# Kernel optimization log

Hardware: AMD Instinct MI355X
Metric: run time of the kernel (lower is better)

## Reference

```python
import jax, jax.numpy as jnp
import numpy as np

FP8_MAX = 448.0  # max finite value of float8_e4m3fn


def setup_inputs() -> dict:
    key = jax.random.key(0)
    k1, k2, k3 = jax.random.split(key, 3)
    B, S, D_IN, D_OUT = 2, 4096, 2048, 8192
    x = jax.random.normal(k1, (B, S, D_IN), dtype=jnp.float32)
    # Weight is stored pre-quantized in fp8 (per-tensor scale), layout (in, out)
    w_fp32 = jax.random.normal(k2, (D_IN, D_OUT), dtype=jnp.float32) * 0.02
    weight_scale = jnp.float32(jnp.max(jnp.abs(w_fp32)) / FP8_MAX)
    weight = jnp.clip(w_fp32 / weight_scale, -FP8_MAX, FP8_MAX).astype(jnp.float8_e4m3fn)
    input_scale = jnp.float32(0.05)  # static per-tensor activation scale
    bias = jax.random.normal(k3, (D_OUT,), dtype=jnp.float32)
    return {"x": x, "weight": weight, "weight_scale": weight_scale,
            "input_scale": input_scale, "bias": bias}


def reference(x, weight, weight_scale, input_scale, bias):
    # static_quantize_e4m3_per_tensor: q = cast_fp8(clip(x / s)), returns (q, s)
    q = jnp.clip(x / input_scale, -FP8_MAX, FP8_MAX).astype(jnp.float8_e4m3fn)
    q2d = q.reshape(-1, q.shape[-1]).astype(jnp.float32)  # [B*S, D_in]
    w = weight.astype(jnp.float32)                         # [D_in, D_out]
    # cublas_scaled_mm: (q @ w) * scale_a * scale_b, out in x.dtype
    out = jnp.matmul(q2d, w) * (input_scale * weight_scale)
    out = out.astype(x.dtype) + bias.astype(x.dtype)
    return out.reshape(x.shape[:-1] + (out.shape[-1],))
```

## Files before the change

kernel.cpp:

```cpp
#include <hip/hip_runtime.h>

typedef __attribute__((ext_vector_type(4))) float floatx4;
typedef __attribute__((ext_vector_type(8))) int   intx8;

__device__ __forceinline__ unsigned int pack4_fp8(float f0, float f1, float f2, float f3) {
    int v = __builtin_amdgcn_cvt_pk_fp8_f32(f0, f1, 0, false);
    v = __builtin_amdgcn_cvt_pk_fp8_f32(f2, f3, v, true);
    return (unsigned int)v;
}

__device__ __forceinline__ void gload16(const unsigned char* g, unsigned char* l) {
    __builtin_amdgcn_global_load_lds(
        (const __attribute__((address_space(1))) unsigned int*)g,
        (__attribute__((address_space(3))) unsigned int*)l, 16, 0, 0);
}

__global__ void detect_kernel(const unsigned int* __restrict__ W, int* __restrict__ flag) {
    __shared__ int ok[2];
    if (threadIdx.x == 0) { ok[0] = 1; ok[1] = 1; }
    __syncthreads();
    int f32ok = 1, bf16ok = 1;
#pragma unroll
    for (int i = 0; i < 16; ++i) {
        unsigned int w = W[threadIdx.x * 16 + i];
        if (w & 0x000FFFFFu) f32ok = 0;
        if (w & 0x000F000Fu) bf16ok = 0;
    }
    if (!f32ok)  atomicAnd(&ok[0], 0);
    if (!bf16ok) atomicAnd(&ok[1], 0);
    __syncthreads();
    if (threadIdx.x == 0) *flag = ok[0] ? 2 : (ok[1] ? 1 : 0);
}

__global__ void quant_kernel(const float* __restrict__ x,
                             unsigned int* __restrict__ q,
                             const float* __restrict__ iscale, int n8) {
    int i = blockIdx.x * blockDim.x + threadIdx.x;
    if (i >= n8) return;
    float s = iscale[0];
    const float4* xv = (const float4*)x;
    float4 a = xv[2 * i];
    float4 b = xv[2 * i + 1];
    float v[8] = {a.x, a.y, a.z, a.w, b.x, b.y, b.z, b.w};
#pragma unroll
    for (int j = 0; j < 8; ++j) {
        float t = v[j] / s;
        v[j] = fminf(fmaxf(t, -448.0f), 448.0f);
    }
    q[2 * i]     = pack4_fp8(v[0], v[1], v[2], v[3]);
    q[2 * i + 1] = pack4_fp8(v[4], v[5], v[6], v[7]);
}

template <int MODE>
__device__ __forceinline__ void ingest_body(const unsigned char* __restrict__ W,
                                            unsigned char* __restrict__ Wt,
                                            int K, int N,
                                            unsigned char (*tile)[68]) {
    const int k0 = blockIdx.y * 64;
    const int n0 = blockIdx.x * 64;
    const int t = threadIdx.x;
    const int kr = t >> 2;
    const int cg = (t & 3) * 16;
    const size_t eidx = (size_t)(k0 + kr) * N + (n0 + cg);

    unsigned int w4[4];
    if constexpr (MODE == 0) {
        uint4 v = *(const uint4*)(W + eidx);
        w4[0] = v.x; w4[1] = v.y; w4[2] = v.z; w4[3] = v.w;
    } else if constexpr (MODE == 1) {
        const uint4* p = (const uint4*)((const unsigned short*)W + eidx);
        uint4 A0 = p[0], A1 = p[1];
        unsigned int uw[8] = {A0.x, A0.y, A0.z, A0.w, A1.x, A1.y, A1.z, A1.w};
#pragma unroll
        for (int g = 0; g < 4; ++g) {
            float f0 = __uint_as_float((uw[2 * g] & 0xFFFFu) << 16);
            float f1 = __uint_as_float((uw[2 * g] >> 16) << 16);
            float f2 = __uint_as_float((uw[2 * g + 1] & 0xFFFFu) << 16);
            float f3 = __uint_as_float((uw[2 * g + 1] >> 16) << 16);
            w4[g] = pack4_fp8(f0, f1, f2, f3);
        }
    } else {
        const float4* p = (const float4*)((const float*)W + eidx);
#pragma unroll
        for (int g = 0; g < 4; ++g) {
            float4 f = p[g];
            w4[g] = pack4_fp8(f.x, f.y, f.z, f.w);
        }
    }
#pragma unroll
    for (int g = 0; g < 4; ++g)
        *(unsigned int*)&tile[kr][cg + 4 * g] = w4[g];
    __syncthreads();

    const int nr = t >> 2;
    const int kg = (t & 3) * 16;
    uint4 o;
    unsigned int w[4];
#pragma unroll
    for (int g = 0; g < 4; ++g) {
        unsigned int b0 = tile[kg + g * 4 + 0][nr];
        unsigned int b1 = tile[kg + g * 4 + 1][nr];
        unsigned int b2 = tile[kg + g * 4 + 2][nr];
        unsigned int b3 = tile[kg + g * 4 + 3][nr];
        w[g] = b0 | (b1 << 8) | (b2 << 16) | (b3 << 24);
    }
    o.x = w[0]; o.y = w[1]; o.z = w[2]; o.w = w[3];
    *(uint4*)(Wt + (size_t)(n0 + nr) * K + k0 + kg) = o;
}

__global__ void ingest_kernel(const unsigned char* __restrict__ W,
                              unsigned char* __restrict__ Wt,
                              const int* __restrict__ flag, int K, int N) {
    __shared__ __align__(16) unsigned char tile[64][68];
    const int mode = *flag;
    if (mode == 0)      ingest_body<0>(W, Wt, K, N, tile);
    else if (mode == 1) ingest_body<1>(W, Wt, K, N, tile);
    else                ingest_body<2>(W, Wt, K, N, tile);
}

__global__ __launch_bounds__(256, 2) void gemm_mxfp8_kernel(
    const unsigned char* __restrict__ A,
    const unsigned char* __restrict__ Bt,
    float* __restrict__ C,
    const float* __restrict__ bias,
    const float* __restrict__ wscale,
    const float* __restrict__ iscale,
    int M, int N, int K) {
    __shared__ __align__(16) unsigned char As[2][16384];
    __shared__ __align__(16) unsigned char Bs[2][16384];

    const int tid  = threadIdx.x;
    const int lane = tid & 63;
    const int wv   = tid >> 6;
    const int wm   = wv >> 1;
    const int wn   = wv & 1;
    const int r16  = lane & 15;
    const int cq   = lane >> 4;

    const int nbx  = gridDim.x;
    const int nwg  = nbx * gridDim.y;
    const int orig = blockIdx.y * nbx + blockIdx.x;
    const int cpx  = nwg >> 3;
    const int swz  = (orig & 7) * cpx + (orig >> 3);
    const int bm   = (swz / nbx) * 128;
    const int bn   = (swz % nbx) * 128;

    const unsigned char* ga[4];
    const unsigned char* gb[4];
    int lo[4];
#pragma unroll
    for (int j = 0; j < 4; ++j) {
        const int u   = wv * 4 + j;
        const int rb  = u >> 1;
        const int rg  = u & 1;
        const int row = rb * 16 + r16;
        const int col = cq * 32 + rg * 16;
        ga[j] = A  + (size_t)(bm + row) * K + col;
        gb[j] = Bt + (size_t)(bn + row) * K + col;
        lo[j] = rb * 2048 + rg * 1024;
    }

    floatx4 acc[4][4] = {};

#pragma unroll
    for (int j = 0; j < 4; ++j) {
        gload16(ga[j], &As[0][lo[j]]);
        gload16(gb[j], &Bs[0][lo[j]]);
        ga[j] += 128; gb[j] += 128;
    }
    __syncthreads();

    const unsigned char* pa0 = &As[0][wm * 4 * 2048 + lane * 16];
    const unsigned char* pb0 = &Bs[0][wn * 4 * 2048 + lane * 16];

    union U8 { intx8 v; uint4 q[2]; };
    const int NT = K >> 7;
    int cur = 0;
    for (int kt = 0; kt < NT; ++kt) {
        if (kt + 1 < NT) {
#pragma unroll
            for (int j = 0; j < 4; ++j) {
                gload16(ga[j], &As[cur ^ 1][lo[j]]);
                gload16(gb[j], &Bs[cur ^ 1][lo[j]]);
                ga[j] += 128; gb[j] += 128;
            }
        }
        intx8 af[4], bf[4];
#pragma unroll
        for (int i = 0; i < 4; ++i) {
            U8 ua, ub;
            const unsigned char* qa = pa0 + cur * 16384 + i * 2048;
            const unsigned char* qb = pb0 + cur * 16384 + i * 2048;
            ua.q[0] = *(const uint4*)qa;
            ua.q[1] = *(const uint4*)(qa + 1024);
            ub.q[0] = *(const uint4*)qb;
            ub.q[1] = *(const uint4*)(qb + 1024);
            af[i] = ua.v;
            bf[i] = ub.v;
        }
#pragma unroll
        for (int im = 0; im < 4; ++im)
#pragma unroll
            for (int in = 0; in < 4; ++in)
                acc[im][in] = __builtin_amdgcn_mfma_scale_f32_16x16x128_f8f6f4(
                    af[im], bf[in], acc[im][in],
                    0, 0,
                    0, 0x7F7F7F7F,
                    0, 0x7F7F7F7F);
        __syncthreads();
        cur ^= 1;
    }
    (void)M;

    const float scale = iscale[0] * wscale[0];
    const int row0 = bm + wm * 64 + (cq << 2);
    const int col0 = bn + wn * 64 + r16;
#pragma unroll
    for (int in = 0; in < 4; ++in) {
        const int col = col0 + in * 16;
        const float bv = bias[col];
#pragma unroll
        for (int im = 0; im < 4; ++im) {
            const int row = row0 + im * 16;
            float* cp = C + (size_t)row * N + col;
#pragma unroll
            for (int r = 0; r < 4; ++r)
                cp[(size_t)r * N] = acc[im][in][r] * scale + bv;
        }
    }
}

extern "C" void kernel_launch(void* const* d_in, const int* in_sizes, int n_in,
                              void* d_out, int out_size, void* d_ws, size_t ws_size,
                              hipStream_t stream) {
    const float* x          = (const float*)d_in[0];
    const unsigned char* w  = (const unsigned char*)d_in[1];
    const float* wscale     = (const float*)d_in[2];
    const float* iscale     = (const float*)d_in[3];
    const float* bias       = (const float*)d_in[4];
    float* out              = (float*)d_out;

    const int D_OUT = in_sizes[4];
    const int D_IN  = in_sizes[1] / D_OUT;
    const int M     = in_sizes[0] / D_IN;

    int* flag         = (int*)d_ws;
    unsigned char* q  = (unsigned char*)d_ws + 256;
    unsigned char* wt = q + (size_t)M * D_IN;

    detect_kernel<<<1, 256, 0, stream>>>((const unsigned int*)w, flag);
    const int n8 = (M * D_IN) / 8;
    quant_kernel<<<(n8 + 255) / 256, 256, 0, stream>>>(x, (unsigned int*)q, iscale, n8);
    dim3 tg(D_OUT / 64, D_IN / 64);
    ingest_kernel<<<tg, 256, 0, stream>>>(w, wt, flag, D_IN, D_OUT);
    gemm_mxfp8_kernel<<<dim3(D_OUT / 128, M / 128), 256, 0, stream>>>(
        q, wt, out, bias, wscale, iscale, M, D_OUT, D_IN);
}
```

Measured before the change: 601.8 us.

## Single-buffer LDS tiles to raise occupancy and drop block swizzle

Replaces the double-buffered LDS staging with a single buffer that is loaded and synchronised at the start of each K step, which halves shared memory per block. The launch bound goes from 2 to 4 blocks per CU so more waves can hide latency. The grouped block-index swizzle is also removed in favour of plain row-major block mapping. In exchange, global-to-LDS loads no longer overlap the MFMA work within a block, the loop now has two barriers per step, and L2 reuse from the swizzle is lost.

```diff
diff --git a/kernel.cpp b/kernel.cpp
--- a/kernel.cpp
+++ b/kernel.cpp
@@ -118,7 +118,7 @@
     else                ingest_body<2>(W, Wt, K, N, tile);
 }
 
-__global__ __launch_bounds__(256, 2) void gemm_mxfp8_kernel(
+__global__ __launch_bounds__(256, 4) void gemm_mxfp8_kernel(
     const unsigned char* __restrict__ A,
     const unsigned char* __restrict__ Bt,
     float* __restrict__ C,
@@ -126,8 +126,8 @@
     const float* __restrict__ wscale,
     const float* __restrict__ iscale,
     int M, int N, int K) {
-    __shared__ __align__(16) unsigned char As[2][16384];
-    __shared__ __align__(16) unsigned char Bs[2][16384];
+    __shared__ __align__(16) unsigned char As[16384];
+    __shared__ __align__(16) unsigned char Bs[16384];
 
     const int tid  = threadIdx.x;
     const int lane = tid & 63;
@@ -137,13 +137,8 @@
     const int r16  = lane & 15;
     const int cq   = lane >> 4;
 
-    const int nbx  = gridDim.x;
-    const int nwg  = nbx * gridDim.y;
-    const int orig = blockIdx.y * nbx + blockIdx.x;
-    const int cpx  = nwg >> 3;
-    const int swz  = (orig & 7) * cpx + (orig >> 3);
-    const int bm   = (swz / nbx) * 128;
-    const int bn   = (swz % nbx) * 128;
+    const int bm = blockIdx.y * 128;
+    const int bn = blockIdx.x * 128;
 
     const unsigned char* ga[4];
     const unsigned char* gb[4];
@@ -162,35 +157,27 @@
 
     floatx4 acc[4][4] = {};
 
-#pragma unroll
-    for (int j = 0; j < 4; ++j) {
-        gload16(ga[j], &As[0][lo[j]]);
-        gload16(gb[j], &Bs[0][lo[j]]);
-        ga[j] += 128; gb[j] += 128;
-    }
-    __syncthreads();
-
-    const unsigned char* pa0 = &As[0][wm * 4 * 2048 + lane * 16];
-    const unsigned char* pb0 = &Bs[0][wn * 4 * 2048 + lane * 16];
+    const unsigned char* pa0 = &As[wm * 4 * 2048 + lane * 16];
+    const unsigned char* pb0 = &Bs[wn * 4 * 2048 + lane * 16];
 
     union U8 { intx8 v; uint4 q[2]; };
     const int NT = K >> 7;
-    int cur = 0;
     for (int kt = 0; kt < NT; ++kt) {
-        if (kt + 1 < NT) {
-#pragma unroll
-            for (int j = 0; j < 4; ++j) {
-                gload16(ga[j], &As[cur ^ 1][lo[j]]);
-                gload16(gb[j], &Bs[cur ^ 1][lo[j]]);
-                ga[j] += 128; gb[j] += 128;
-            }
-        }
+        __syncthreads();
+#pragma unroll
+        for (int j = 0; j < 4; ++j) {
+            gload16(ga[j], &As[lo[j]]);
+            gload16(gb[j], &Bs[lo[j]]);
+            ga[j] += 128; gb[j] += 128;
+        }
+        __syncthreads();
+
         intx8 af[4], bf[4];
 #pragma unroll
         for (int i = 0; i < 4; ++i) {
             U8 ua, ub;
-            const unsigned char* qa = pa0 + cur * 16384 + i * 2048;
-            const unsigned char* qb = pb0 + cur * 16384 + i * 2048;
+            const unsigned char* qa = pa0 + i * 2048;
+            const unsigned char* qb = pb0 + i * 2048;
             ua.q[0] = *(const uint4*)qa;
             ua.q[1] = *(const uint4*)(qa + 1024);
             ub.q[0] = *(const uint4*)qb;
@@ -207,8 +194,6 @@
                     0, 0,
                     0, 0x7F7F7F7F,
                     0, 0x7F7F7F7F);
-        __syncthreads();
-        cur ^= 1;
     }
     (void)M;
 
```

New measurement: 571.0 us. 1.05x faster.
